# Kernel tuning notes

Hardware: AMD Instinct MI355X
Metric: run time of the kernel (lower is better)

Reference implementation:

```python
import jax, jax.numpy as jnp
import numpy as np

N = 50000
E = 600000
D_IN = 128
D_HID = 128
D_OUT = 40
BN_EPS = 1e-5


def setup_inputs() -> dict:
    key = jax.random.key(0)
    ks = jax.random.split(key, 16)
    g = lambda k, *s: (jax.random.normal(k, s, jnp.float32) * 0.05)
    return {
        "x": jax.random.normal(ks[0], (N, D_IN), jnp.float32),
        "edge_index": jax.random.randint(ks[1], (2, E), 0, N, dtype=jnp.int64),
        "W0": g(ks[2], D_IN, D_HID), "b0": jnp.zeros((D_HID,), jnp.float32),
        "W1": g(ks[3], D_HID, D_HID), "b1": jnp.zeros((D_HID,), jnp.float32),
        "W2": g(ks[4], D_HID, D_OUT), "b2": jnp.zeros((D_OUT,), jnp.float32),
        "g0": 1.0 + g(ks[5], D_HID), "be0": g(ks[6], D_HID),
        "m0": g(ks[7], D_HID), "v0": 0.5 + jax.random.uniform(ks[8], (D_HID,), jnp.float32),
        "g1": 1.0 + g(ks[9], D_HID), "be1": g(ks[10], D_HID),
        "m1": g(ks[11], D_HID), "v1": 0.5 + jax.random.uniform(ks[12], (D_HID,), jnp.float32),
    }


def reference(x, edge_index, W0, b0, W1, b1, W2, b2,
              g0, be0, m0, v0, g1, be1, m1, v1):
    n = x.shape[0]
    loop = jnp.arange(n, dtype=edge_index.dtype)
    # GCN with self-loops: A_hat = A + I, symmetric normalization
    src = jnp.concatenate([edge_index[0], loop])
    dst = jnp.concatenate([edge_index[1], loop])
    deg = jax.ops.segment_sum(jnp.ones_like(dst, jnp.float32), dst, num_segments=n)
    dinv = jax.lax.rsqrt(jnp.maximum(deg, 1.0))
    norm = dinv[src] * dinv[dst]  # [E+N]

    def conv(h, W, b):
        h = h @ W + b                                   # [N, d_out]
        msg = norm[:, None] * h[src]                    # gather + scale
        return jax.ops.segment_sum(msg, dst, num_segments=n)

    def bn_relu(h, g, be, m, v):
        return jax.nn.relu((h - m) * (g * jax.lax.rsqrt(v + BN_EPS)) + be)

    h = bn_relu(conv(x, W0, b0), g0, be0, m0, v0)
    h = bn_relu(conv(h, W1, b1), g1, be1, m1, v1)
    h = conv(h, W2, b2)
    return jax.nn.log_softmax(h, axis=-1)
```

## Files before the change

kernel.cpp:

```cpp
#include <hip/hip_runtime.h>
#include <math.h>

#define BN_EPS 1e-5f
#define CAP 96

typedef unsigned short ushort_t;
typedef __attribute__((ext_vector_type(8))) short short8;
typedef __attribute__((ext_vector_type(4))) float floatx4;

__device__ inline ushort_t f2b(float f) {
    unsigned u = __float_as_uint(f);
    unsigned r = u + 0x7FFFu + ((u >> 16) & 1u);
    return (ushort_t)(r >> 16);
}
__device__ inline float b2f(ushort_t b) { return __uint_as_float(((unsigned)b) << 16); }
__device__ inline float2 u2f2(unsigned u) {
    return make_float2(b2f((ushort_t)(u & 0xffffu)), b2f((ushort_t)(u >> 16)));
}

__global__ __launch_bounds__(256) void fill_ell_cast(
    const int* __restrict__ ei, int* __restrict__ cnt, ushort_t* __restrict__ ell,
    const float* __restrict__ W0, const float* __restrict__ W1, const float* __restrict__ W2,
    ushort_t* __restrict__ Wt0, ushort_t* __restrict__ Wt1, ushort_t* __restrict__ Wt2,
    int E, int FB)
{
    int bid = blockIdx.x;
    if (bid < FB) {
        int e = bid * 256 + threadIdx.x;
        if (e < E) {
            int s = ei[e];
            int d = ei[E + e];
            int p = atomicAdd(&cnt[d], 1);
            if (p < CAP) ell[(size_t)d * CAP + p] = (ushort_t)s;
        }
        return;
    }
    int i = (bid - FB) * 256 + threadIdx.x;
    if (i < 16384) {
        int n = i >> 7, k = i & 127;
        Wt0[i] = f2b(W0[k * 128 + n]);
    } else if (i < 32768) {
        int j = i - 16384;
        int n = j >> 7, k = j & 127;
        Wt1[j] = f2b(W1[k * 128 + n]);
    } else if (i < 40960) {
        int j = i - 32768;
        int n = j >> 7, k = j & 127;
        Wt2[j] = (n < 40) ? f2b(W2[k * 40 + n]) : (ushort_t)0;
    }
}

__global__ void make_dinv(const int* __restrict__ cnt, float* __restrict__ dinv, int n) {
    int i = blockIdx.x * blockDim.x + threadIdx.x;
    if (i < n) dinv[i] = rsqrtf((float)(cnt[i] + 1));
}

template<int NT, bool AF32>
__global__ __launch_bounds__(256) void gemm_mfma(const void* __restrict__ Av,
                                                 const ushort_t* __restrict__ Wt,
                                                 const float* __restrict__ bias,
                                                 const float* __restrict__ dinv,
                                                 ushort_t* __restrict__ C,
                                                 int M, int ncols) {
    __shared__ ushort_t Ws[NT * 128];
    const int tid = threadIdx.x;
    const int rbase = blockIdx.x * 128;

#pragma unroll
    for (int p = 0; p < NT / 16; ++p) {
        int cid = p * 256 + tid;
        int nr = cid >> 4, seg = cid & 15;
        *(uint4*)(Ws + nr * 128 + ((seg ^ (nr & 15)) << 3)) =
            *(const uint4*)(Wt + (size_t)cid * 8);
    }
    __syncthreads();

    const int wave = tid >> 6, lane = tid & 63;
    const int m = lane & 15, quad = lane >> 4;
    constexpr int CT = NT / 16;
    floatx4 acc[2][CT];
#pragma unroll
    for (int rt = 0; rt < 2; ++rt)
#pragma unroll
        for (int ct = 0; ct < CT; ++ct) acc[rt][ct] = (floatx4){0.f, 0.f, 0.f, 0.f};

    const int r0 = wave * 32;
    const int ra = rbase + r0 + m;
    const int rb = ra + 16;
    const bool oka = ra < M, okb = rb < M;

#pragma unroll
    for (int ks = 0; ks < 4; ++ks) {
        int ko = ks * 32 + quad * 8;
        short8 a0 = {0, 0, 0, 0, 0, 0, 0, 0}, a1 = a0;
        if (AF32) {
            const float* A32 = (const float*)Av;
            if (oka) {
                const float* p = A32 + (size_t)ra * 128 + ko;
                float4 f0 = *(const float4*)p, f1 = *(const float4*)(p + 4);
                a0[0] = f2b(f0.x); a0[1] = f2b(f0.y); a0[2] = f2b(f0.z); a0[3] = f2b(f0.w);
                a0[4] = f2b(f1.x); a0[5] = f2b(f1.y); a0[6] = f2b(f1.z); a0[7] = f2b(f1.w);
            }
            if (okb) {
                const float* p = A32 + (size_t)rb * 128 + ko;
                float4 f0 = *(const float4*)p, f1 = *(const float4*)(p + 4);
                a1[0] = f2b(f0.x); a1[1] = f2b(f0.y); a1[2] = f2b(f0.z); a1[3] = f2b(f0.w);
                a1[4] = f2b(f1.x); a1[5] = f2b(f1.y); a1[6] = f2b(f1.z); a1[7] = f2b(f1.w);
            }
        } else {
            const ushort_t* A16 = (const ushort_t*)Av;
            if (oka) a0 = *(const short8*)(A16 + (size_t)ra * 128 + ko);
            if (okb) a1 = *(const short8*)(A16 + (size_t)rb * 128 + ko);
        }
#pragma unroll
        for (int ct = 0; ct < CT; ++ct) {
            short8 b = *(const short8*)(Ws + (ct * 16 + m) * 128 + (((ks * 4 + quad) ^ m) << 3));
            acc[0][ct] = __builtin_amdgcn_mfma_f32_16x16x32_bf16(a0, b, acc[0][ct], 0, 0, 0);
            acc[1][ct] = __builtin_amdgcn_mfma_f32_16x16x32_bf16(a1, b, acc[1][ct], 0, 0, 0);
        }
    }

    float dsc[2][4];
#pragma unroll
    for (int rt = 0; rt < 2; ++rt)
#pragma unroll
        for (int r = 0; r < 4; ++r) {
            int gr = rbase + r0 + rt * 16 + quad * 4 + r;
            dsc[rt][r] = (gr < M) ? dinv[gr] : 0.f;
        }

    __syncthreads();
    constexpr int SEGN = NT / 8, CMASK = SEGN - 1;
#pragma unroll
    for (int rt = 0; rt < 2; ++rt)
#pragma unroll
        for (int ct = 0; ct < CT; ++ct) {
            int col = ct * 16 + m;
            float bv = (col < ncols) ? bias[col] : 0.f;
            int seg = col >> 3, cl = col & 7;
#pragma unroll
            for (int r = 0; r < 4; ++r) {
                int row = r0 + rt * 16 + quad * 4 + r;
                Ws[row * NT + ((seg ^ (row & CMASK)) << 3) + cl] =
                    f2b((acc[rt][ct][r] + bv) * dsc[rt][r]);
            }
        }
    __syncthreads();
    constexpr int CPT = (128 * SEGN) / 256;
#pragma unroll
    for (int p = 0; p < CPT; ++p) {
        int cid = p * 256 + tid;
        int row = cid / SEGN, seg = cid & CMASK;
        int gr = rbase + row;
        if (gr < M)
            *(uint4*)(C + (size_t)gr * NT + seg * 8) =
                *(const uint4*)(Ws + row * NT + ((seg ^ (row & CMASK)) << 3));
    }
}

__global__ __launch_bounds__(256) void agg128_bn(const ushort_t* __restrict__ h,
                                                 const int* __restrict__ cnt,
                                                 const ushort_t* __restrict__ ell,
                                                 const float* __restrict__ dinv,
                                                 const float* __restrict__ g,
                                                 const float* __restrict__ be,
                                                 const float* __restrict__ mB,
                                                 const float* __restrict__ v,
                                                 ushort_t* __restrict__ out, int n) {
    int wv = __builtin_amdgcn_readfirstlane((blockIdx.x * 256 + threadIdx.x) >> 6);
    int lane = threadIdx.x & 63;
    if (wv >= n) return;
    const unsigned* h2 = (const unsigned*)h;
    float dv = dinv[wv];
    float2 hv = u2f2(h2[(size_t)wv * 64 + lane]);
    float ax = hv.x, ay = hv.y;
    int c = min(cnt[wv], CAP);
    const ushort_t* row = ell + (size_t)wv * CAP;
    int k = 0;
    for (; k + 8 <= c; k += 8) {
        int s[8];
#pragma unroll
        for (int j = 0; j < 8; ++j) s[j] = row[k + j];
#pragma unroll
        for (int j = 0; j < 8; ++j) {
            float2 t = u2f2(h2[(size_t)s[j] * 64 + lane]);
            ax += t.x;
            ay += t.y;
        }
    }
    if (k < c) {
        int rem = c - k;
        int s[8];
#pragma unroll
        for (int j = 0; j < 8; ++j) {
            int sr = row[k + j];
            s[j] = (j < rem) ? sr : 0;
        }
#pragma unroll
        for (int j = 0; j < 8; ++j) {
            float2 t = u2f2(h2[(size_t)s[j] * 64 + lane]);
            ax += (j < rem) ? t.x : 0.f;
            ay += (j < rem) ? t.y : 0.f;
        }
    }
    ax *= dv;
    ay *= dv;
    int c0 = lane * 2;
    float s0f = g[c0] * rsqrtf(v[c0] + BN_EPS);
    float s1f = g[c0 + 1] * rsqrtf(v[c0 + 1] + BN_EPS);
    float o0 = fmaxf(fmaf(ax - mB[c0], s0f, be[c0]), 0.f);
    float o1 = fmaxf(fmaf(ay - mB[c0 + 1], s1f, be[c0 + 1]), 0.f);
    unsigned ov = (unsigned)f2b(o0) | ((unsigned)f2b(o1) << 16);
    ((unsigned*)out)[(size_t)wv * 64 + lane] = ov;
}

__global__ __launch_bounds__(256) void agg40_lsm(const ushort_t* __restrict__ h,
                                                 const int* __restrict__ cnt,
                                                 const ushort_t* __restrict__ ell,
                                                 const float* __restrict__ dinv,
                                                 float* __restrict__ out, int n) {
    int wv = __builtin_amdgcn_readfirstlane((blockIdx.x * 256 + threadIdx.x) >> 6);
    int lane = threadIdx.x & 63;
    if (wv >= n) return;
    float dv = dinv[wv];
    float acc = b2f(h[(size_t)wv * 64 + lane]);
    int c = min(cnt[wv], CAP);
    const ushort_t* row = ell + (size_t)wv * CAP;
    int k = 0;
    for (; k + 8 <= c; k += 8) {
        int s[8];
#pragma unroll
        for (int j = 0; j < 8; ++j) s[j] = row[k + j];
#pragma unroll
        for (int j = 0; j < 8; ++j) acc += b2f(h[(size_t)s[j] * 64 + lane]);
    }
    if (k < c) {
        int rem = c - k;
        int s[8];
#pragma unroll
        for (int j = 0; j < 8; ++j) {
            int sr = row[k + j];
            s[j] = (j < rem) ? sr : 0;
        }
#pragma unroll
        for (int j = 0; j < 8; ++j) {
            float t = b2f(h[(size_t)s[j] * 64 + lane]);
            acc += (j < rem) ? t : 0.f;
        }
    }
    acc *= dv;
    bool act = lane < 40;
    float x = act ? acc : -INFINITY;
    float mx = x;
#pragma unroll
    for (int off = 32; off > 0; off >>= 1) mx = fmaxf(mx, __shfl_xor(mx, off, 64));
    float ex = act ? expf(acc - mx) : 0.f;
    float se = ex;
#pragma unroll
    for (int off = 32; off > 0; off >>= 1) se += __shfl_xor(se, off, 64);
    float r = acc - mx - logf(se);
    if (act) out[(size_t)wv * 40 + lane] = r;
}


extern "C" void kernel_launch(void* const* d_in, const int* in_sizes, int n_in,
                              void* d_out, int out_size, void* d_ws, size_t ws_size,
                              hipStream_t stream) {
    const float* x = (const float*)d_in[0];
    const int* ei = (const int*)d_in[1];
    const float* W0 = (const float*)d_in[2];
    const float* b0 = (const float*)d_in[3];
    const float* W1 = (const float*)d_in[4];
    const float* b1 = (const float*)d_in[5];
    const float* W2 = (const float*)d_in[6];
    const float* b2 = (const float*)d_in[7];
    const float* g0 = (const float*)d_in[8];
    const float* be0 = (const float*)d_in[9];
    const float* m0 = (const float*)d_in[10];
    const float* v0 = (const float*)d_in[11];
    const float* g1 = (const float*)d_in[12];
    const float* be1 = (const float*)d_in[13];
    const float* m1 = (const float*)d_in[14];
    const float* v1 = (const float*)d_in[15];
    float* out = (float*)d_out;

    const int N = in_sizes[0] / 128;
    const int E = in_sizes[1] / 2;

    char* wp = (char*)d_ws;
    auto alloc = [&](size_t bytes) -> char* {
        char* p = wp;
        wp += (bytes + 255) & ~(size_t)255;
        return p;
    };
    int* cnt = (int*)alloc((size_t)N * 4);
    float* dinv = (float*)alloc((size_t)N * 4);
    ushort_t* ell = (ushort_t*)alloc(((size_t)N * CAP + 16) * 2);
    ushort_t* hA = (ushort_t*)alloc((size_t)N * 128 * 2);
    ushort_t* hB = (ushort_t*)alloc((size_t)N * 128 * 2);
    ushort_t* hA2 = (ushort_t*)alloc((size_t)N * 128 * 2);
    ushort_t* hB2 = (ushort_t*)alloc((size_t)N * 128 * 2);
    ushort_t* hL = (ushort_t*)alloc((size_t)N * 64 * 2);
    ushort_t* Wt0 = (ushort_t*)alloc(128 * 128 * 2);
    ushort_t* Wt1 = (ushort_t*)alloc(128 * 128 * 2);
    ushort_t* Wt2 = (ushort_t*)alloc(64 * 128 * 2);

    const int GB = (N + 127) / 128;
    const int FB = (E + 255) / 256;
    const int CB = 160;

    hipMemsetAsync(cnt, 0, (size_t)N * 4, stream);
    fill_ell_cast<<<FB + CB, 256, 0, stream>>>(ei, cnt, ell, W0, W1, W2,
                                               Wt0, Wt1, Wt2, E, FB);
    make_dinv<<<(N + 255) / 256, 256, 0, stream>>>(cnt, dinv, N);

    gemm_mfma<128, true><<<GB, 256, 0, stream>>>(x, Wt0, b0, dinv, hA, N, 128);
    agg128_bn<<<(N + 3) / 4, 256, 0, stream>>>(hA, cnt, ell, dinv, g0, be0, m0, v0, hB, N);
    gemm_mfma<128, false><<<GB, 256, 0, stream>>>(hB, Wt1, b1, dinv, hA2, N, 128);
    agg128_bn<<<(N + 3) / 4, 256, 0, stream>>>(hA2, cnt, ell, dinv, g1, be1, m1, v1, hB2, N);
    gemm_mfma<64, false><<<GB, 256, 0, stream>>>(hB2, Wt2, b2, dinv, hL, N, 40);
    agg40_lsm<<<(N + 3) / 4, 256, 0, stream>>>(hL, cnt, ell, dinv, out, N);
}
```

Baseline: 231.8 us.

## Fuse aggregation+BN+ReLU with next GEMM and compute dinv inline

Merges each hidden-layer aggregation (gather, BN, ReLU) with the following MFMA GEMM. The aggregated rows go into a swizzled LDS tile and are multiplied by the next weight matrix in the same kernel, so the intermediate hB/hB2 buffers no longer make a round trip through global memory. The separate make_dinv kernel is removed and rsqrt(cnt+1) is recomputed wherever it is needed. ELL indices are now read as uint4 vectors, and the GEMM kernels gain grid-stride tile loops. The trade-offs are the loss of wave-per-row parallelism in the gather, since each wave now processes 16 rows serially, and higher LDS use per block.

```diff
diff --git a/kernel.cpp b/kernel.cpp
--- a/kernel.cpp
+++ b/kernel.cpp
@@ -18,7 +18,25 @@
     return make_float2(b2f((ushort_t)(u & 0xffffu)), b2f((ushort_t)(u >> 16)));
 }
 
-__global__ __launch_bounds__(256) void fill_ell_cast(
+__device__ inline void cast_weights(const float* __restrict__ W0, const float* __restrict__ W1,
+                                    const float* __restrict__ W2, ushort_t* __restrict__ Wt0,
+                                    ushort_t* __restrict__ Wt1, ushort_t* __restrict__ Wt2,
+                                    int i) {
+    if (i < 16384) {
+        int nn = i >> 7, k = i & 127;
+        Wt0[i] = f2b(W0[k * 128 + nn]);
+    } else if (i < 32768) {
+        int j = i - 16384;
+        int nn = j >> 7, k = j & 127;
+        Wt1[j] = f2b(W1[k * 128 + nn]);
+    } else if (i < 40960) {
+        int j = i - 32768;
+        int nn = j >> 7, k = j & 127;
+        Wt2[j] = (nn < 40) ? f2b(W2[k * 40 + nn]) : (ushort_t)0;
+    }
+}
+
+__global__ __launch_bounds__(256) void k_fill_cast(
     const int* __restrict__ ei, int* __restrict__ cnt, ushort_t* __restrict__ ell,
     const float* __restrict__ W0, const float* __restrict__ W1, const float* __restrict__ W2,
     ushort_t* __restrict__ Wt0, ushort_t* __restrict__ Wt1, ushort_t* __restrict__ Wt2,
@@ -35,104 +53,229 @@
         }
         return;
     }
-    int i = (bid - FB) * 256 + threadIdx.x;
-    if (i < 16384) {
-        int n = i >> 7, k = i & 127;
-        Wt0[i] = f2b(W0[k * 128 + n]);
-    } else if (i < 32768) {
-        int j = i - 16384;
-        int n = j >> 7, k = j & 127;
-        Wt1[j] = f2b(W1[k * 128 + n]);
-    } else if (i < 40960) {
-        int j = i - 32768;
-        int n = j >> 7, k = j & 127;
-        Wt2[j] = (n < 40) ? f2b(W2[k * 40 + n]) : (ushort_t)0;
-    }
-}
-
-__global__ void make_dinv(const int* __restrict__ cnt, float* __restrict__ dinv, int n) {
-    int i = blockIdx.x * blockDim.x + threadIdx.x;
-    if (i < n) dinv[i] = rsqrtf((float)(cnt[i] + 1));
+    cast_weights(W0, W1, W2, Wt0, Wt1, Wt2, (bid - FB) * 256 + threadIdx.x);
 }
 
 template<int NT, bool AF32>
-__global__ __launch_bounds__(256) void gemm_mfma(const void* __restrict__ Av,
-                                                 const ushort_t* __restrict__ Wt,
-                                                 const float* __restrict__ bias,
-                                                 const float* __restrict__ dinv,
-                                                 ushort_t* __restrict__ C,
-                                                 int M, int ncols) {
+__global__ __launch_bounds__(256) void k_gemm(const void* __restrict__ Av,
+                                              const ushort_t* __restrict__ Wt,
+                                              const float* __restrict__ bias,
+                                              const int* __restrict__ cnt,
+                                              ushort_t* __restrict__ C,
+                                              int M, int ncols) {
     __shared__ ushort_t Ws[NT * 128];
     const int tid = threadIdx.x;
-    const int rbase = blockIdx.x * 128;
-
-#pragma unroll
-    for (int p = 0; p < NT / 16; ++p) {
-        int cid = p * 256 + tid;
-        int nr = cid >> 4, seg = cid & 15;
-        *(uint4*)(Ws + nr * 128 + ((seg ^ (nr & 15)) << 3)) =
-            *(const uint4*)(Wt + (size_t)cid * 8);
-    }
-    __syncthreads();
-
+    const int ntiles = (M + 127) >> 7;
     const int wave = tid >> 6, lane = tid & 63;
     const int m = lane & 15, quad = lane >> 4;
     constexpr int CT = NT / 16;
-    floatx4 acc[2][CT];
-#pragma unroll
-    for (int rt = 0; rt < 2; ++rt)
-#pragma unroll
-        for (int ct = 0; ct < CT; ++ct) acc[rt][ct] = (floatx4){0.f, 0.f, 0.f, 0.f};
-
     const int r0 = wave * 32;
-    const int ra = rbase + r0 + m;
-    const int rb = ra + 16;
-    const bool oka = ra < M, okb = rb < M;
-
-#pragma unroll
-    for (int ks = 0; ks < 4; ++ks) {
-        int ko = ks * 32 + quad * 8;
-        short8 a0 = {0, 0, 0, 0, 0, 0, 0, 0}, a1 = a0;
-        if (AF32) {
-            const float* A32 = (const float*)Av;
-            if (oka) {
-                const float* p = A32 + (size_t)ra * 128 + ko;
-                float4 f0 = *(const float4*)p, f1 = *(const float4*)(p + 4);
-                a0[0] = f2b(f0.x); a0[1] = f2b(f0.y); a0[2] = f2b(f0.z); a0[3] = f2b(f0.w);
-                a0[4] = f2b(f1.x); a0[5] = f2b(f1.y); a0[6] = f2b(f1.z); a0[7] = f2b(f1.w);
-            }
-            if (okb) {
-                const float* p = A32 + (size_t)rb * 128 + ko;
-                float4 f0 = *(const float4*)p, f1 = *(const float4*)(p + 4);
-                a1[0] = f2b(f0.x); a1[1] = f2b(f0.y); a1[2] = f2b(f0.z); a1[3] = f2b(f0.w);
-                a1[4] = f2b(f1.x); a1[5] = f2b(f1.y); a1[6] = f2b(f1.z); a1[7] = f2b(f1.w);
-            }
-        } else {
-            const ushort_t* A16 = (const ushort_t*)Av;
-            if (oka) a0 = *(const short8*)(A16 + (size_t)ra * 128 + ko);
-            if (okb) a1 = *(const short8*)(A16 + (size_t)rb * 128 + ko);
-        }
-#pragma unroll
-        for (int ct = 0; ct < CT; ++ct) {
-            short8 b = *(const short8*)(Ws + (ct * 16 + m) * 128 + (((ks * 4 + quad) ^ m) << 3));
-            acc[0][ct] = __builtin_amdgcn_mfma_f32_16x16x32_bf16(a0, b, acc[0][ct], 0, 0, 0);
-            acc[1][ct] = __builtin_amdgcn_mfma_f32_16x16x32_bf16(a1, b, acc[1][ct], 0, 0, 0);
-        }
-    }
-
-    float dsc[2][4];
-#pragma unroll
-    for (int rt = 0; rt < 2; ++rt)
+
+    for (int t = blockIdx.x; t < ntiles; t += gridDim.x) {
+        const int rbase = t << 7;
+#pragma unroll
+        for (int p = 0; p < NT / 16; ++p) {
+            int cid = p * 256 + tid;
+            int nr = cid >> 4, seg = cid & 15;
+            *(uint4*)(Ws + nr * 128 + ((seg ^ (nr & 15)) << 3)) =
+                *(const uint4*)(Wt + (size_t)cid * 8);
+        }
+        __syncthreads();
+
+        floatx4 acc[2][CT];
+#pragma unroll
+        for (int rt = 0; rt < 2; ++rt)
+#pragma unroll
+            for (int ct = 0; ct < CT; ++ct) acc[rt][ct] = (floatx4){0.f, 0.f, 0.f, 0.f};
+
+        const int ra = rbase + r0 + m;
+        const int rb = ra + 16;
+        const bool oka = ra < M, okb = rb < M;
+
+#pragma unroll
+        for (int ks = 0; ks < 4; ++ks) {
+            int ko = ks * 32 + quad * 8;
+            short8 a0 = {0, 0, 0, 0, 0, 0, 0, 0}, a1 = a0;
+            if (AF32) {
+                const float* A32 = (const float*)Av;
+                if (oka) {
+                    const float* p = A32 + (size_t)ra * 128 + ko;
+                    float4 f0 = *(const float4*)p, f1 = *(const float4*)(p + 4);
+                    a0[0] = f2b(f0.x); a0[1] = f2b(f0.y); a0[2] = f2b(f0.z); a0[3] = f2b(f0.w);
+                    a0[4] = f2b(f1.x); a0[5] = f2b(f1.y); a0[6] = f2b(f1.z); a0[7] = f2b(f1.w);
+                }
+                if (okb) {
+                    const float* p = A32 + (size_t)rb * 128 + ko;
+                    float4 f0 = *(const float4*)p, f1 = *(const float4*)(p + 4);
+                    a1[0] = f2b(f0.x); a1[1] = f2b(f0.y); a1[2] = f2b(f0.z); a1[3] = f2b(f0.w);
+                    a1[4] = f2b(f1.x); a1[5] = f2b(f1.y); a1[6] = f2b(f1.z); a1[7] = f2b(f1.w);
+                }
+            } else {
+                const ushort_t* A16 = (const ushort_t*)Av;
+                if (oka) a0 = *(const short8*)(A16 + (size_t)ra * 128 + ko);
+                if (okb) a1 = *(const short8*)(A16 + (size_t)rb * 128 + ko);
+            }
+#pragma unroll
+            for (int ct = 0; ct < CT; ++ct) {
+                short8 b = *(const short8*)(Ws + (ct * 16 + m) * 128 + (((ks * 4 + quad) ^ m) << 3));
+                acc[0][ct] = __builtin_amdgcn_mfma_f32_16x16x32_bf16(a0, b, acc[0][ct], 0, 0, 0);
+                acc[1][ct] = __builtin_amdgcn_mfma_f32_16x16x32_bf16(a1, b, acc[1][ct], 0, 0, 0);
+            }
+        }
+
+        float dsc[2][4];
+#pragma unroll
+        for (int rt = 0; rt < 2; ++rt)
+#pragma unroll
+            for (int r = 0; r < 4; ++r) {
+                int gr = rbase + r0 + rt * 16 + quad * 4 + r;
+                dsc[rt][r] = (gr < M) ? rsqrtf((float)(cnt[gr] + 1)) : 0.f;
+            }
+
+        __syncthreads();
+        constexpr int SEGN = NT / 8, CMASK = SEGN - 1;
+#pragma unroll
+        for (int rt = 0; rt < 2; ++rt)
+#pragma unroll
+            for (int ct = 0; ct < CT; ++ct) {
+                int col = ct * 16 + m;
+                float bv = (col < ncols) ? bias[col] : 0.f;
+                int seg = col >> 3, cl = col & 7;
+#pragma unroll
+                for (int r = 0; r < 4; ++r) {
+                    int row = r0 + rt * 16 + quad * 4 + r;
+                    Ws[row * NT + ((seg ^ (row & CMASK)) << 3) + cl] =
+                        f2b((acc[rt][ct][r] + bv) * dsc[rt][r]);
+                }
+            }
+        __syncthreads();
+        constexpr int CPT = (128 * SEGN) / 256;
+#pragma unroll
+        for (int p = 0; p < CPT; ++p) {
+            int cid = p * 256 + tid;
+            int row = cid / SEGN, seg = cid & CMASK;
+            int gr = rbase + row;
+            if (gr < M)
+                *(uint4*)(C + (size_t)gr * NT + seg * 8) =
+                    *(const uint4*)(Ws + row * NT + ((seg ^ (row & CMASK)) << 3));
+        }
+        __syncthreads();
+    }
+}
+
+template<int NT>
+__global__ __launch_bounds__(256) void fused_ag(
+    const ushort_t* __restrict__ h,
+    const int* __restrict__ cnt,
+    const ushort_t* __restrict__ ell,
+    const float* __restrict__ g, const float* __restrict__ be,
+    const float* __restrict__ mB, const float* __restrict__ v,
+    const ushort_t* __restrict__ Wt,
+    const float* __restrict__ bias,
+    ushort_t* __restrict__ C,
+    int M, int ncols)
+{
+    __shared__ ushort_t As[64 * 128];
+    __shared__ ushort_t Ws[NT * 128];
+    const int tid = threadIdx.x;
+    const int ntiles = (M + 63) >> 6;
+    const int wave = tid >> 6, lane = tid & 63;
+    const int m = lane & 15, quad = lane >> 4;
+    constexpr int CT = NT / 16;
+    const int r0 = wave * 16;
+    const unsigned* h2 = (const unsigned*)h;
+    unsigned* As2 = (unsigned*)As;
+
+    const int c0 = lane * 2;
+    const float s0f = g[c0] * rsqrtf(v[c0] + BN_EPS);
+    const float s1f = g[c0 + 1] * rsqrtf(v[c0 + 1] + BN_EPS);
+    const float m0v = mB[c0], m1v = mB[c0 + 1], b0v = be[c0], b1v = be[c0 + 1];
+
+    for (int t = blockIdx.x; t < ntiles; t += gridDim.x) {
+        const int rbase = t << 6;
+
+#pragma unroll
+        for (int p = 0; p < NT / 16; ++p) {
+            int cid = p * 256 + tid;
+            int nr = cid >> 4, seg = cid & 15;
+            *(uint4*)(Ws + nr * 128 + ((seg ^ (nr & 15)) << 3)) =
+                *(const uint4*)(Wt + (size_t)cid * 8);
+        }
+
+        for (int rr = 0; rr < 16; ++rr) {
+            const int rl = r0 + rr;
+            const int gr = rbase + rl;
+            unsigned ov = 0;
+            if (gr < M) {
+                int cd = cnt[gr];
+                float dv = rsqrtf((float)(cd + 1));
+                float2 hv = u2f2(h2[(size_t)gr * 64 + lane]);
+                float ax = hv.x, ay = hv.y;
+                int c = min(cd, CAP);
+                const uint4* rowv = (const uint4*)(ell + (size_t)gr * CAP);
+                int k = 0;
+                for (; k + 8 <= c; k += 8) {
+                    uint4 iv = rowv[k >> 3];
+                    int s[8] = {(int)(iv.x & 0xffffu), (int)(iv.x >> 16),
+                                (int)(iv.y & 0xffffu), (int)(iv.y >> 16),
+                                (int)(iv.z & 0xffffu), (int)(iv.z >> 16),
+                                (int)(iv.w & 0xffffu), (int)(iv.w >> 16)};
+#pragma unroll
+                    for (int j = 0; j < 8; ++j) {
+                        float2 tt = u2f2(h2[(size_t)s[j] * 64 + lane]);
+                        ax += tt.x;
+                        ay += tt.y;
+                    }
+                }
+                if (k < c) {
+                    int rem = c - k;
+                    uint4 iv = rowv[k >> 3];
+                    int sr[8] = {(int)(iv.x & 0xffffu), (int)(iv.x >> 16),
+                                 (int)(iv.y & 0xffffu), (int)(iv.y >> 16),
+                                 (int)(iv.z & 0xffffu), (int)(iv.z >> 16),
+                                 (int)(iv.w & 0xffffu), (int)(iv.w >> 16)};
+                    int s[8];
+#pragma unroll
+                    for (int j = 0; j < 8; ++j) s[j] = (j < rem) ? sr[j] : 0;
+#pragma unroll
+                    for (int j = 0; j < 8; ++j) {
+                        float2 tt = u2f2(h2[(size_t)s[j] * 64 + lane]);
+                        ax += (j < rem) ? tt.x : 0.f;
+                        ay += (j < rem) ? tt.y : 0.f;
+                    }
+                }
+                ax *= dv;
+                ay *= dv;
+                float o0 = fmaxf(fmaf(ax - m0v, s0f, b0v), 0.f);
+                float o1 = fmaxf(fmaf(ay - m1v, s1f, b1v), 0.f);
+                ov = (unsigned)f2b(o0) | ((unsigned)f2b(o1) << 16);
+            }
+            As2[rl * 64 + (((lane >> 2) ^ (rl & 15)) << 2) + (lane & 3)] = ov;
+        }
+        __syncthreads();
+
+        floatx4 acc[CT];
+#pragma unroll
+        for (int ct = 0; ct < CT; ++ct) acc[ct] = (floatx4){0.f, 0.f, 0.f, 0.f};
+#pragma unroll
+        for (int ks = 0; ks < 4; ++ks) {
+            short8 a0 = *(const short8*)(As + (r0 + m) * 128 + (((ks * 4 + quad) ^ m) << 3));
+#pragma unroll
+            for (int ct = 0; ct < CT; ++ct) {
+                short8 b = *(const short8*)(Ws + (ct * 16 + m) * 128 + (((ks * 4 + quad) ^ m) << 3));
+                acc[ct] = __builtin_amdgcn_mfma_f32_16x16x32_bf16(a0, b, acc[ct], 0, 0, 0);
+            }
+        }
+
+        float dsc[4];
 #pragma unroll
         for (int r = 0; r < 4; ++r) {
-            int gr = rbase + r0 + rt * 16 + quad * 4 + r;
-            dsc[rt][r] = (gr < M) ? dinv[gr] : 0.f;
-        }
-
-    __syncthreads();
-    constexpr int SEGN = NT / 8, CMASK = SEGN - 1;
-#pragma unroll
-    for (int rt = 0; rt < 2; ++rt)
+            int gr2 = rbase + r0 + quad * 4 + r;
+            dsc[r] = (gr2 < M) ? rsqrtf((float)(cnt[gr2] + 1)) : 0.f;
+        }
+
+        __syncthreads();
+        constexpr int SEGN = NT / 8, CMASK = SEGN - 1;
 #pragma unroll
         for (int ct = 0; ct < CT; ++ct) {
             int col = ct * 16 + m;
@@ -140,41 +283,37 @@
             int seg = col >> 3, cl = col & 7;
 #pragma unroll
             for (int r = 0; r < 4; ++r) {
-                int row = r0 + rt * 16 + quad * 4 + r;
-                Ws[row * NT + ((seg ^ (row & CMASK)) << 3) + cl] =
-                    f2b((acc[rt][ct][r] + bv) * dsc[rt][r]);
-            }
-        }
-    __syncthreads();
-    constexpr int CPT = (128 * SEGN) / 256;
-#pragma unroll
-    for (int p = 0; p < CPT; ++p) {
-        int cid = p * 256 + tid;
-        int row = cid / SEGN, seg = cid & CMASK;
-        int gr = rbase + row;
-        if (gr < M)
-            *(uint4*)(C + (size_t)gr * NT + seg * 8) =
-                *(const uint4*)(Ws + row * NT + ((seg ^ (row & CMASK)) << 3));
-    }
-}
-
-__global__ __launch_bounds__(256) void agg128_bn(const ushort_t* __restrict__ h,
-                                                 const int* __restrict__ cnt,
-                                                 const ushort_t* __restrict__ ell,
-                                                 const float* __restrict__ dinv,
-                                                 const float* __restrict__ g,
-                                                 const float* __restrict__ be,
-                                                 const float* __restrict__ mB,
-                                                 const float* __restrict__ v,
-                                                 ushort_t* __restrict__ out, int n) {
+                int row = r0 + quad * 4 + r;
+                As[row * NT + ((seg ^ (row & CMASK)) << 3) + cl] =
+                    f2b((acc[ct][r] + bv) * dsc[r]);
+            }
+        }
+        __syncthreads();
+        constexpr int CPT = (64 * SEGN) / 256;
+#pragma unroll
+        for (int p = 0; p < CPT; ++p) {
+            int cid = p * 256 + tid;
+            int row = cid / SEGN, seg = cid & CMASK;
+            int gr = rbase + row;
+            if (gr < M)
+                *(uint4*)(C + (size_t)gr * NT + seg * 8) =
+                    *(const uint4*)(As + row * NT + ((seg ^ (row & CMASK)) << 3));
+        }
+        __syncthreads();
+    }
+}
+
+__global__ __launch_bounds__(256) void k_agg40(const ushort_t* __restrict__ h,
+                                               const int* __restrict__ cnt,
+                                               const ushort_t* __restrict__ ell,
+                                               float* __restrict__ out, int n) {
     int wv = __builtin_amdgcn_readfirstlane((blockIdx.x * 256 + threadIdx.x) >> 6);
     int lane = threadIdx.x & 63;
     if (wv >= n) return;
-    const unsigned* h2 = (const unsigned*)h;
-    float dv = dinv[wv];
-    float2 hv = u2f2(h2[(size_t)wv * 64 + lane]);
-    float ax = hv.x, ay = hv.y;
-    int c = min(cnt[wv], CAP);
+    int cd = cnt[wv];
+    float dv = rsqrtf((float)(cd + 1));
+    float acc = b2f(h[(size_t)wv * 64 + lane]);
+    int c = min(cd, CAP);
     const ushort_t* row = ell + (size_t)wv * CAP;
     int k = 0;
     for (; k + 8 <= c; k += 8) {
@@ -182,11 +321,7 @@
 #pragma unroll
         for (int j = 0; j < 8; ++j) s[j] = row[k + j];
 #pragma unroll
-        for (int j = 0; j < 8; ++j) {
-            float2 t = u2f2(h2[(size_t)s[j] * 64 + lane]);
-            ax += t.x;
-            ay += t.y;
-        }
+        for (int j = 0; j < 8; ++j) acc += b2f(h[(size_t)s[j] * 64 + lane]);
     }
     if (k < c) {
         int rem = c - k;
@@ -198,60 +333,14 @@
         }
 #pragma unroll
         for (int j = 0; j < 8; ++j) {
-            float2 t = u2f2(h2[(size_t)s[j] * 64 + lane]);
-            ax += (j < rem) ? t.x : 0.f;
-            ay += (j < rem) ? t.y : 0.f;
-        }
-    }
-    ax *= dv;
-    ay *= dv;
-    int c0 = lane * 2;
-    float s0f = g[c0] * rsqrtf(v[c0] + BN_EPS);
-    float s1f = g[c0 + 1] * rsqrtf(v[c0 + 1] + BN_EPS);
-    float o0 = fmaxf(fmaf(ax - mB[c0], s0f, be[c0]), 0.f);
-    float o1 = fmaxf(fmaf(ay - mB[c0 + 1], s1f, be[c0 + 1]), 0.f);
-    unsigned ov = (unsigned)f2b(o0) | ((unsigned)f2b(o1) << 16);
-    ((unsigned*)out)[(size_t)wv * 64 + lane] = ov;
-}
-
-__global__ __launch_bounds__(256) void agg40_lsm(const ushort_t* __restrict__ h,
-                                                 const int* __restrict__ cnt,
-                                                 const ushort_t* __restrict__ ell,
-                                                 const float* __restrict__ dinv,
-                                                 float* __restrict__ out, int n) {
-    int wv = __builtin_amdgcn_readfirstlane((blockIdx.x * 256 + threadIdx.x) >> 6);
-    int lane = threadIdx.x & 63;
-    if (wv >= n) return;
-    float dv = dinv[wv];
-    float acc = b2f(h[(size_t)wv * 64 + lane]);
-    int c = min(cnt[wv], CAP);
-    const ushort_t* row = ell + (size_t)wv * CAP;
-    int k = 0;
-    for (; k + 8 <= c; k += 8) {
-        int s[8];
-#pragma unroll
-        for (int j = 0; j < 8; ++j) s[j] = row[k + j];
-#pragma unroll
-        for (int j = 0; j < 8; ++j) acc += b2f(h[(size_t)s[j] * 64 + lane]);
-    }
-    if (k < c) {
-        int rem = c - k;
-        int s[8];
-#pragma unroll
-        for (int j = 0; j < 8; ++j) {
-            int sr = row[k + j];
-            s[j] = (j < rem) ? sr : 0;
-        }
-#pragma unroll
-        for (int j = 0; j < 8; ++j) {
             float t = b2f(h[(size_t)s[j] * 64 + lane]);
             acc += (j < rem) ? t : 0.f;
         }
     }
     acc *= dv;
     bool act = lane < 40;
-    float x = act ? acc : -INFINITY;
-    float mx = x;
+    float xv = act ? acc : -INFINITY;
+    float mx = xv;
 #pragma unroll
     for (int off = 32; off > 0; off >>= 1) mx = fmaxf(mx, __shfl_xor(mx, off, 64));
     float ex = act ? expf(acc - mx) : 0.f;
@@ -294,30 +383,26 @@
         return p;
     };
     int* cnt = (int*)alloc((size_t)N * 4);
-    float* dinv = (float*)alloc((size_t)N * 4);
     ushort_t* ell = (ushort_t*)alloc(((size_t)N * CAP + 16) * 2);
     ushort_t* hA = (ushort_t*)alloc((size_t)N * 128 * 2);
-    ushort_t* hB = (ushort_t*)alloc((size_t)N * 128 * 2);
     ushort_t* hA2 = (ushort_t*)alloc((size_t)N * 128 * 2);
-    ushort_t* hB2 = (ushort_t*)alloc((size_t)N * 128 * 2);
     ushort_t* hL = (ushort_t*)alloc((size_t)N * 64 * 2);
     ushort_t* Wt0 = (ushort_t*)alloc(128 * 128 * 2);
     ushort_t* Wt1 = (ushort_t*)alloc(128 * 128 * 2);
     ushort_t* Wt2 = (ushort_t*)alloc(64 * 128 * 2);
 
     const int GB = (N + 127) / 128;
+    const int TG = (N + 63) / 64;
     const int FB = (E + 255) / 256;
     const int CB = 160;
 
     hipMemsetAsync(cnt, 0, (size_t)N * 4, stream);
-    fill_ell_cast<<<FB + CB, 256, 0, stream>>>(ei, cnt, ell, W0, W1, W2,
-                                               Wt0, Wt1, Wt2, E, FB);
-    make_dinv<<<(N + 255) / 256, 256, 0, stream>>>(cnt, dinv, N);
-
-    gemm_mfma<128, true><<<GB, 256, 0, stream>>>(x, Wt0, b0, dinv, hA, N, 128);
-    agg128_bn<<<(N + 3) / 4, 256, 0, stream>>>(hA, cnt, ell, dinv, g0, be0, m0, v0, hB, N);
-    gemm_mfma<128, false><<<GB, 256, 0, stream>>>(hB, Wt1, b1, dinv, hA2, N, 128);
-    agg128_bn<<<(N + 3) / 4, 256, 0, stream>>>(hA2, cnt, ell, dinv, g1, be1, m1, v1, hB2, N);
-    gemm_mfma<64, false><<<GB, 256, 0, stream>>>(hB2, Wt2, b2, dinv, hL, N, 40);
-    agg40_lsm<<<(N + 3) / 4, 256, 0, stream>>>(hL, cnt, ell, dinv, out, N);
-}
+    k_fill_cast<<<FB + CB, 256, 0, stream>>>(ei, cnt, ell, W0, W1, W2,
+                                             Wt0, Wt1, Wt2, E, FB);
+    k_gemm<128, true><<<GB, 256, 0, stream>>>(x, Wt0, b0, cnt, hA, N, 128);
+    fused_ag<128><<<TG, 256, 0, stream>>>(hA, cnt, ell, g0, be0, m0, v0,
+                                          Wt1, b1, hA2, N, 128);
+    fused_ag<64><<<TG, 256, 0, stream>>>(hA2, cnt, ell, g1, be1, m1, v1,
+                                         Wt2, b2, hL, N, 40);
+    k_agg40<<<(N + 3) / 4, 256, 0, stream>>>(hL, cnt, ell, out, N);
+}
```

Measured after the change: 277.4 us. 1.2x slower.
